# Kernel optimization log

Hardware: AMD Instinct MI355X
Metric: run time of the kernel (lower is better)

The kernel has to match this reference:

```python
import jax, jax.numpy as jnp
import numpy as np
import math

D_MODEL = 1024
D_INNER = 2048
N_HEADS = 8
D_STATE = 64
D_CONV = 4
CHUNK = 64
HEAD_DIM = D_INNER // N_HEADS
EPS = 1.1920929e-07  # torch RMSNorm default eps = finfo(fp32).eps


def _rms(x, g):
    return x * jax.lax.rsqrt(jnp.mean(x * x, axis=-1, keepdims=True) + EPS) * g


def setup_inputs() -> dict:
    key = jax.random.key(0)
    ks = jax.random.split(key, 8)
    B, S = 32, 256
    proj_out = 2 * D_INNER + 2 * N_HEADS * D_STATE + N_HEADS  # 5128
    s = 0.02
    lambdas = [0.999, 0.995, 0.99, 0.98, 0.95, 0.9, 0.8, 0.7]
    A_log = jnp.log(jnp.asarray([-math.log(l) for l in lambdas], jnp.float32))
    return {
        "hidden": jax.random.normal(ks[0], (B, S, D_MODEL), jnp.float32),
        "W_in": jax.random.normal(ks[1], (proj_out, D_MODEL), jnp.float32) * s,
        "conv_w": jax.random.normal(ks[2], (D_INNER, 1, D_CONV), jnp.float32) * 0.2,
        "conv_b": jax.random.normal(ks[3], (D_INNER,), jnp.float32) * 0.02,
        "W_dt": jax.random.normal(ks[4], (D_INNER, N_HEADS), jnp.float32) * 0.1,
        "b_dt": jax.random.normal(ks[5], (D_INNER,), jnp.float32) * 0.1,
        "A_log": A_log,
        "D": jnp.ones((N_HEADS,), jnp.float32),
        "W_out": jax.random.normal(ks[6], (D_MODEL, D_INNER), jnp.float32) * s,
        "g_in": jnp.ones((D_MODEL,), jnp.float32),
        "g_out": jnp.ones((D_INNER,), jnp.float32),
    }


def reference(hidden, W_in, conv_w, conv_b, W_dt, b_dt, A_log, D, W_out, g_in, g_out):
    B, S, _ = hidden.shape
    residual = hidden
    h = _rms(hidden, g_in)
    proj = h @ W_in.T  # [B,S,5128]
    o1, o2 = D_INNER, 2 * D_INNER
    o3 = o2 + N_HEADS * D_STATE
    o4 = o3 + N_HEADS * D_STATE
    z = proj[..., :o1]
    x = proj[..., o1:o2]
    Bf = proj[..., o2:o3]
    Cf = proj[..., o3:o4]
    dt_raw = proj[..., o4:]
    # causal depthwise conv1d (pad left d_conv-1, trim to S)
    xt = jnp.transpose(x, (0, 2, 1))  # [B, d_inner, S]
    xc = jax.lax.conv_general_dilated(
        xt, conv_w, (1,), [(D_CONV - 1, 0)],
        feature_group_count=D_INNER, dimension_numbers=("NCH", "OIH", "NCH"))
    x = jax.nn.silu(jnp.transpose(xc + conv_b[None, :, None], (0, 2, 1)))
    # dt: project 8 -> d_inner then mean over head_dim -> per-head dt
    dt = dt_raw @ W_dt.T + b_dt  # [B,S,d_inner]
    dt_h = jax.nn.softplus(dt.reshape(B, S, N_HEADS, HEAD_DIM).mean(-1))  # non-TTT path (S<384)
    Bs = Bf.reshape(B, S, N_HEADS, D_STATE)
    Cs = Cf.reshape(B, S, N_HEADS, D_STATE)
    x_h = x.reshape(B, S, N_HEADS, HEAD_DIM)
    # chunked SSD scan
    A = -jnp.exp(A_log)  # [H]
    nC, L = S // CHUNK, CHUNK
    xck = x_h.reshape(B, nC, L, N_HEADS, HEAD_DIM)
    Bck = Bs.reshape(B, nC, L, N_HEADS, D_STATE)
    Cck = Cs.reshape(B, nC, L, N_HEADS, D_STATE)
    logA = dt_h.reshape(B, nC, L, N_HEADS) * A  # [B,c,L,H]
    lcs = jnp.cumsum(logA, axis=2)
    lcs_t = jnp.transpose(lcs, (0, 1, 3, 2))  # [B,c,H,L]
    tril = jnp.tril(jnp.ones((L, L), bool))
    M = jnp.where(tril, jnp.exp(lcs_t[..., :, None] - lcs_t[..., None, :]), 0.0)  # [B,c,H,L,L]
    # intra-chunk: sum_{s<=l,n} C[l,n] M[l,s] B[s,n] x[s,d]
    G = jnp.einsum("bclhn,bcshn->bchls", Cck, Bck)
    intra = jnp.einsum("bchls,bcshd->bclhd", G * M, xck)
    # per-chunk state contributions and decays
    Mlast = jnp.exp(lcs_t[..., -1:] - lcs_t)  # [B,c,H,L] decay from step s to chunk end
    states = jnp.einsum("bchs,bcshn,bcshd->bchdn", Mlast, Bck, xck)  # [B,c,H,hD,N]
    tdec = jnp.exp(lcs[:, :, -1, :])  # [B,c,H]
    def step(hst, inp):
        td, st = inp
        return td[..., None, None] * hst + st, hst
    init = jnp.zeros((B, N_HEADS, HEAD_DIM, D_STATE), x.dtype)
    _, h0 = jax.lax.scan(step, init, (jnp.moveaxis(tdec, 1, 0), jnp.moveaxis(states, 1, 0)))
    # inter-chunk: decay(l) * C[l] . h_start
    inter = jnp.exp(lcs)[..., None] * jnp.einsum("bclhn,cbhdn->bclhd", Cck, h0)
    y = (intra + inter).reshape(B, S, N_HEADS, HEAD_DIM) + x_h * D[None, None, :, None]
    y = y.reshape(B, S, D_INNER) * jax.nn.silu(z)
    y = _rms(y, g_out)
    return residual + y @ W_out.T
```

## Files before the change

kernel.cpp:

```cpp
#include <hip/hip_runtime.h>
#include <hip/hip_bf16.h>
#include <math.h>

typedef __hip_bfloat16 bf16;
typedef __attribute__((ext_vector_type(8))) short short8;
typedef __attribute__((ext_vector_type(4))) float f32x4;

#define AS1 __attribute__((address_space(1)))
#define AS3 __attribute__((address_space(3)))

#define D_MODEL 1024
#define D_INNER 2048
#define N_HEADS 8
#define D_STATE 64
#define CHUNK 64
#define HEAD_DIM 256
#define NCHUNK 4
#define BATCH 32
#define SEQ 256
#define ROWS (BATCH*SEQ)
#define PROJ_N 5128
#define PROJ_NPAD 5376
#define O1 D_INNER
#define O2 (2*D_INNER)
#define O3 (O2 + N_HEADS*D_STATE)
#define O4 (O3 + N_HEADS*D_STATE)
#define EPSF 1.1920929e-07f

__device__ __forceinline__ float silu_f(float x){ return x / (1.0f + expf(-x)); }
__device__ __forceinline__ float b2f(bf16 v){ return __bfloat162float(v); }
__device__ __forceinline__ bf16  f2b(float v){ return __float2bfloat16(v); }
__device__ __forceinline__ short f2s(float v){ bf16 b = __float2bfloat16(v); union{bf16 b; short s;} u; u.b=b; return u.s; }
__device__ __forceinline__ float s2f(short v){ union{short s; bf16 b;} u; u.s=v; return __bfloat162float(u.b); }

__device__ __forceinline__ void gl16(const void* g, void* l){
    __builtin_amdgcn_global_load_lds((const AS1 void*)g, (AS3 void*)l, 16, 0, 0);
}

__device__ __forceinline__ float block_sum_256(float v){
    __shared__ float sm[4];
    #pragma unroll
    for (int o = 32; o > 0; o >>= 1) v += __shfl_down(v, o, 64);
    int lane = threadIdx.x & 63, w = threadIdx.x >> 6;
    if (lane == 0) sm[w] = v;
    __syncthreads();
    return sm[0] + sm[1] + sm[2] + sm[3];
}

__global__ __launch_bounds__(256) void k_rms_in(const float* __restrict__ x,
                                                const float* __restrict__ g,
                                                bf16* __restrict__ out){
    int row = blockIdx.x, t = threadIdx.x;
    const float4* xr = (const float4*)(x + (size_t)row * D_MODEL);
    float4 v = xr[t];
    float ss = v.x*v.x + v.y*v.y + v.z*v.z + v.w*v.w;
    ss = block_sum_256(ss);
    float sc = rsqrtf(ss * (1.0f/(float)D_MODEL) + EPSF);
    float4 gv = ((const float4*)g)[t];
    union { ushort4 u; bf16 b[4]; } o;
    o.b[0] = f2b(v.x*sc*gv.x); o.b[1] = f2b(v.y*sc*gv.y);
    o.b[2] = f2b(v.z*sc*gv.z); o.b[3] = f2b(v.w*sc*gv.w);
    ((ushort4*)(out + (size_t)row * D_MODEL))[t] = o.u;
}

#define N1 (PROJ_NPAD*D_MODEL)
__global__ __launch_bounds__(256) void k_cvt_both(const float* __restrict__ W_in,
                                                  const float* __restrict__ W_out,
                                                  const float* __restrict__ g_out,
                                                  bf16* __restrict__ Wb1,
                                                  bf16* __restrict__ Wb2){
    int i = (blockIdx.x * 256 + threadIdx.x) * 4;
    union { ushort4 u; bf16 b[4]; } o;
    if (i < N1){
        int n_in = PROJ_N*D_MODEL;
        if (i + 3 < n_in){
            float4 v = *(const float4*)(W_in + i);
            o.b[0]=f2b(v.x); o.b[1]=f2b(v.y); o.b[2]=f2b(v.z); o.b[3]=f2b(v.w);
        } else {
            #pragma unroll
            for (int j = 0; j < 4; j++) o.b[j] = f2b((i+j < n_in) ? W_in[i+j] : 0.f);
        }
        *(ushort4*)(Wb1 + i) = o.u;
    } else {
        int k2 = i - N1;
        if (k2 < D_MODEL*D_INNER){
            float4 v = *(const float4*)(W_out + k2);
            float4 gv = *(const float4*)(g_out + (k2 & (D_INNER-1)));
            o.b[0]=f2b(v.x*gv.x); o.b[1]=f2b(v.y*gv.y); o.b[2]=f2b(v.z*gv.z); o.b[3]=f2b(v.w*gv.w);
            *(ushort4*)(Wb2 + k2) = o.u;
        }
    }
}


__device__ __forceinline__ short8 ld32(const short* base, int row, int g){
    int sr = row >> 1;
    int e8 = (((row & 1) << 2) | g) ^ (sr & 7);
    return *(const short8*)(base + sr*64 + e8*8);
}

__device__ __forceinline__ void stage_u(const bf16* __restrict__ Ag,
                                        const bf16* __restrict__ Bg,
                                        int K, size_t bm, size_t bn, int t,
                                        short* buf, int j){
    const int tid = threadIdx.x;
    const int wid = tid >> 6;
    int cidx = j*512 + tid;
    int srow = cidx >> 3, s8 = cidx & 7;
    int eff = s8 ^ (srow & 7);
    int grow = srow*2 + (eff >> 2);
    int gcol = t*32 + (eff & 3)*8;
    const bf16* src = (grow < 256)
        ? Ag + (bm + grow) * (size_t)K + gcol
        : Bg + (bn + grow - 256) * (size_t)K + gcol;
    gl16(src, buf + (size_t)(j*512 + wid*64)*8);
}

#define MFMA_BF16(A_,B_,C_) __builtin_amdgcn_mfma_f32_16x16x32_bf16(A_,B_,C_,0,0,0)

__device__ __forceinline__ void gemm_main(const bf16* __restrict__ Ag,
                                          const bf16* __restrict__ Bg,
                                          int K, size_t bm, size_t bn,
                                          short* lds, f32x4 (&acc)[4][4]){
    constexpr int TILE = 384*32;
    const int NT = K >> 5;
    const int lane = threadIdx.x & 63;
    const int wid = threadIdx.x >> 6;
    const int wm = wid >> 1, wn = wid & 1;
    const int fr = lane & 15, g = lane >> 4;

    #pragma unroll
    for (int j = 0; j < 3; j++) stage_u(Ag, Bg, K, bm, bn, 0, lds, j);
    #pragma unroll
    for (int j = 0; j < 3; j++) stage_u(Ag, Bg, K, bm, bn, 1, lds + TILE, j);
    asm volatile("s_waitcnt vmcnt(3)" ::: "memory");
    __builtin_amdgcn_sched_barrier(0);
    __builtin_amdgcn_s_barrier();
    __builtin_amdgcn_sched_barrier(0);

    int cur = 0;
    for (int t = 0; t < NT; t++){
        short* buf = lds + cur*TILE;
        int sg = cur + 2; if (sg >= 3) sg -= 3;
        short* stg = lds + sg*TILE;
        short8 a[4], b[4];
        #pragma unroll
        for (int m = 0; m < 4; m++) a[m] = ld32(buf, wm*64 + m*16 + fr, g);
        #pragma unroll
        for (int n = 0; n < 4; n++) b[n] = ld32(buf, 256 + wn*64 + n*16 + fr, g);
        if (t + 2 < NT){
            stage_u(Ag, Bg, K, bm, bn, t+2, stg, 0);
            stage_u(Ag, Bg, K, bm, bn, t+2, stg, 1);
            stage_u(Ag, Bg, K, bm, bn, t+2, stg, 2);
        }
        __builtin_amdgcn_s_setprio(1);
        #pragma unroll
        for (int m = 0; m < 4; m++)
            #pragma unroll
            for (int n = 0; n < 4; n++)
                acc[m][n] = MFMA_BF16(a[m], b[n], acc[m][n]);
        __builtin_amdgcn_s_setprio(0);
        __builtin_amdgcn_sched_barrier(0);
        if (t + 2 < NT)      asm volatile("s_waitcnt vmcnt(3)" ::: "memory");
        else if (t + 1 < NT) asm volatile("s_waitcnt vmcnt(0)" ::: "memory");
        __builtin_amdgcn_sched_barrier(0);
        __builtin_amdgcn_s_barrier();
        __builtin_amdgcn_sched_barrier(0);
        cur = cur + 1 == 3 ? 0 : cur + 1;
    }
}

__global__ __launch_bounds__(512, 4) void k_gemm1_g(const bf16* __restrict__ A,
                                                    const bf16* __restrict__ B,
                                                    bf16* __restrict__ z,
                                                    bf16* __restrict__ xp,
                                                    bf16* __restrict__ Bc,
                                                    bf16* __restrict__ Cc,
                                                    float* __restrict__ dtr){
    extern __shared__ short lds[];
    int wg = (blockIdx.x & 7)*168 + (blockIdx.x >> 3);
    int grp = wg / 192, rem = wg % 192;
    int nt_ = grp*6 + rem % 6;
    int mt_ = rem / 6;
    size_t bm = (size_t)mt_ * 256;
    size_t bn = (size_t)nt_ * 128;
    f32x4 acc[4][4] = {};
    gemm_main(A, B, D_MODEL, bm, bn, lds, acc);
    const int lane = threadIdx.x & 63;
    const int wid = threadIdx.x >> 6;
    const int wm = wid >> 1, wn = wid & 1;
    int cr = (lane >> 4)*4, cc = lane & 15;
    #pragma unroll
    for (int m = 0; m < 4; m++){
        size_t r0 = bm + wm*64 + m*16 + cr;
        #pragma unroll
        for (int n = 0; n < 4; n++){
            int c = (int)bn + wn*64 + n*16 + cc;
            #pragma unroll
            for (int j = 0; j < 4; j++){
                float v = acc[m][n][j];
                size_t r = r0 + j;
                if (c < O1)            z  [r * D_INNER + c]        = f2b(v);
                else if (c < O2)       xp [r * D_INNER + (c - O1)] = f2b(v);
                else if (c < O3)       Bc [r * 512 + (c - O2)]     = f2b(v);
                else if (c < O4)       Cc [r * 512 + (c - O3)]     = f2b(v);
                else if (c < PROJ_N)   dtr[r * 8 + (c - O4)]       = v;
            }
        }
    }
}

__global__ __launch_bounds__(512, 4) void k_gemm2_g(const bf16* __restrict__ A,
                                                    const bf16* __restrict__ B,
                                                    const float* __restrict__ res,
                                                    float* __restrict__ C){
    extern __shared__ short lds[];
    int wg = (blockIdx.x & 7)*32 + (blockIdx.x >> 3);
    size_t bm = (size_t)(wg >> 3) * 256;
    size_t bn = (size_t)(wg & 7) * 128;
    f32x4 acc[4][4] = {};
    gemm_main(A, B, D_INNER, bm, bn, lds, acc);
    const int lane = threadIdx.x & 63;
    const int wid = threadIdx.x >> 6;
    const int wm = wid >> 1, wn = wid & 1;
    int cr = (lane >> 4)*4, cc = lane & 15;
    #pragma unroll
    for (int m = 0; m < 4; m++){
        size_t r0 = bm + wm*64 + m*16 + cr;
        #pragma unroll
        for (int n = 0; n < 4; n++){
            size_t c = bn + wn*64 + n*16 + cc;
            #pragma unroll
            for (int j = 0; j < 4; j++){
                size_t r = r0 + j;
                C[r * D_MODEL + c] = acc[m][n][j] + res[r * D_MODEL + c];
            }
        }
    }
}

__global__ __launch_bounds__(256) void k_conv_silu(const bf16* __restrict__ xp,
                                                   const float* __restrict__ cw,
                                                   const float* __restrict__ cb,
                                                   bf16* __restrict__ xout){
    int b = blockIdx.x;
    int c = blockIdx.y * 256 + threadIdx.x;
    int s0 = blockIdx.z * 32;
    float w0 = cw[c*4+0], w1 = cw[c*4+1], w2 = cw[c*4+2], w3 = cw[c*4+3];
    float bias = cb[c];
    const bf16* ib = xp + (size_t)b * SEQ * D_INNER + c;
    bf16* ob = xout + (size_t)b * SEQ * D_INNER + c;
    float x0 = 0.f, x1 = 0.f, x2 = 0.f;
    if (s0 >= 3){
        x0 = b2f(ib[(size_t)(s0-3) * D_INNER]);
        x1 = b2f(ib[(size_t)(s0-2) * D_INNER]);
        x2 = b2f(ib[(size_t)(s0-1) * D_INNER]);
    }
    #pragma unroll 4
    for (int s = s0; s < s0 + 32; s++){
        float x3 = b2f(ib[(size_t)s * D_INNER]);
        float a = x0*w0 + x1*w1 + x2*w2 + x3*w3 + bias;
        ob[(size_t)s * D_INNER] = f2b(silu_f(a));
        x0 = x1; x1 = x2; x2 = x3;
    }
}

__global__ __launch_bounds__(64) void k_dt_lcs(const float* __restrict__ dtr,
                                               const float* __restrict__ W_dt,
                                               const float* __restrict__ b_dt,
                                               const float* __restrict__ A_log,
                                               float* __restrict__ lcs,
                                               float* __restrict__ tdec){
    __shared__ float sm[80];
    __shared__ float la[CHUNK][N_HEADS];
    int bc = blockIdx.x;
    int l = threadIdx.x;
    {
        int h = l >> 3, k = l & 7;
        float s = 0.f;
        for (int d = 0; d < HEAD_DIM; d++) s += W_dt[(size_t)(h*HEAD_DIM + d) * N_HEADS + k];
        sm[l] = s * (1.0f/(float)HEAD_DIM);
        if (l < 8){
            float sb = 0.f;
            for (int d = 0; d < HEAD_DIM; d++) sb += b_dt[l*HEAD_DIM + d];
            sm[64 + l] = sb * (1.0f/(float)HEAD_DIM);
            sm[72 + l] = -expf(A_log[l]);
        }
    }
    __syncthreads();
    const float* dr = dtr + (size_t)(bc*CHUNK + l) * 8;
    float d0 = dr[0], d1 = dr[1], d2 = dr[2], d3 = dr[3];
    float d4 = dr[4], d5 = dr[5], d6 = dr[6], d7 = dr[7];
    #pragma unroll
    for (int h = 0; h < 8; h++){
        float dt = sm[64+h]
                 + d0*sm[h*8+0] + d1*sm[h*8+1] + d2*sm[h*8+2] + d3*sm[h*8+3]
                 + d4*sm[h*8+4] + d5*sm[h*8+5] + d6*sm[h*8+6] + d7*sm[h*8+7];
        float sp = (dt > 20.f) ? dt : log1pf(expf(dt));
        la[l][h] = sp * sm[72+h];
    }
    __syncthreads();
    float out[8];
    #pragma unroll
    for (int h = 0; h < 8; h++) out[h] = 0.f;
    for (int l2 = 0; l2 <= l; l2++){
        #pragma unroll
        for (int h = 0; h < 8; h++) out[h] += la[l2][h];
    }
    float* lo = lcs + (size_t)(bc*CHUNK + l) * N_HEADS;
    #pragma unroll
    for (int h = 0; h < 8; h++) lo[h] = out[h];
    if (l == 63){
        #pragma unroll
        for (int h = 0; h < 8; h++) tdec[bc*N_HEADS + h] = expf(out[h]);
    }
}

#define LB   0
#define LC   4096
#define LGM  8192
#define LXT  12800
#define LSH  29184
#define LF   45568
#define LDS_BYTES 91904

__device__ __forceinline__ short8 frag_sw(const short* arr, int r, int k){
    return *(const short8*)(arr + r*64 + (k ^ ((r&7)<<3)));
}

__global__ __launch_bounds__(256, 1) void k_ssm(const bf16* __restrict__ Bc,
                                                const bf16* __restrict__ Cc,
                                                bf16* xg,
                                                const float* __restrict__ lcs,
                                                const float* __restrict__ tdec,
                                                const float* __restrict__ Dv){
    extern __shared__ short lds[];
    short* Blds  = lds + LB;
    short* Clds  = lds + LC;
    short* GMlds = lds + LGM;
    short* XTlds = lds + LXT;
    short* Shr   = lds + LSH;
    float* el = (float*)(lds + LF);
    float* ml = el + 64;
    float* ee = el + 128;

    const int tid = threadIdx.x;
    const int lane = tid & 63;
    const int wid = tid >> 6;
    const int fr = lane & 15;
    const int fk = (lane >> 4) * 8;
    const int r0 = (lane >> 4) * 4;
    const int b = blockIdx.x >> 3, h = blockIdx.x & 7;
    const float Dh = Dv[h];

    f32x4 carry[4][4] = {};

    for (int c = 0; c < NCHUNK; c++){
        const int bc = b*NCHUNK + c;
        __syncthreads();
        #pragma unroll
        for (int i = 0; i < 2; i++){
            int slot = i*256 + tid;
            int s = slot >> 3, u = slot & 7;
            size_t rb = (size_t)(bc*CHUNK + s) * 512 + h*64 + ((u ^ (s&7)) * 8);
            gl16(Bc + rb, Blds + slot*8);
            gl16(Cc + rb, Clds + slot*8);
        }
        #pragma unroll
        for (int i = 0; i < 8; i++){
            int slot = i*256 + tid;
            int s = slot >> 5, ck = slot & 31;
            gl16(xg + (size_t)(bc*CHUNK + s) * D_INNER + h*HEAD_DIM + ck*8, Shr + slot*8);
        }
        if (tid < 64) el[tid] = lcs[(size_t)(bc*CHUNK + tid) * N_HEADS + h];
        __syncthreads();
        if (tid < 64){
            float e63 = el[63];
            ml[tid] = expf(e63 - el[tid]);
            ee[tid] = expf(el[tid]);
        }
        #pragma unroll
        for (int i = 0; i < 8; i++){
            short8 t8;
            #pragma unroll
            for (int j = 0; j < 8; j++) t8[j] = Shr[(i*8 + j)*HEAD_DIM + tid];
            *(short8*)(XTlds + tid*64 + ((i*8) ^ ((tid&7)<<3))) = t8;
        }
        __syncthreads();
        {
            f32x4 accg[4] = {};
            #pragma unroll
            for (int kk = 0; kk < 2; kk++){
                short8 a = frag_sw(Clds, wid*16 + fr, kk*32 + fk);
                #pragma unroll
                for (int nt = 0; nt < 4; nt++){
                    short8 bb = frag_sw(Blds, nt*16 + fr, kk*32 + fk);
                    accg[nt] = __builtin_amdgcn_mfma_f32_16x16x32_bf16(a, bb, accg[nt], 0, 0, 0);
                }
            }
            #pragma unroll
            for (int nt = 0; nt < 4; nt++){
                int s = nt*16 + fr;
                float els = el[s];
                #pragma unroll
                for (int j = 0; j < 4; j++){
                    int l = wid*16 + r0 + j;
                    float f = (s <= l) ? expf(el[l] - els) : 0.f;
                    GMlds[l*72 + s] = f2s(accg[nt][j] * f);
                }
            }
            int crow = wid*16 + (lane >> 2), cq = lane & 3;
            float fe = ee[crow];
            #pragma unroll
            for (int half = 0; half < 2; half++){
                short8 v = *(short8*)(Clds + crow*64 + cq*16 + half*8);
                #pragma unroll
                for (int j = 0; j < 8; j++) v[j] = f2s(s2f(v[j]) * fe);
                *(short8*)(Clds + crow*64 + cq*16 + half*8) = v;
            }
        }
        #pragma unroll
        for (int mt = 0; mt < 4; mt++)
            #pragma unroll
            for (int nt = 0; nt < 4; nt++)
                #pragma unroll
                for (int j = 0; j < 4; j++){
                    int d = wid*64 + mt*16 + r0 + j;
                    int n = nt*16 + fr;
                    Shr[d*64 + (n ^ ((d&7)<<3))] = f2s(carry[mt][nt][j]);
                }
        float btv[16];
        {
            int bn_ = tid & 63, bq = tid >> 6;
            #pragma unroll
            for (int i = 0; i < 16; i++){
                int s = bq*16 + i;
                btv[i] = s2f(Blds[s*64 + (bn_ ^ ((s&7)<<3))]) * ml[s];
            }
        }
        __syncthreads();
        {
            int bn_ = tid & 63, bq = tid >> 6;
            #pragma unroll
            for (int i = 0; i < 16; i++){
                int s = bq*16 + i;
                Blds[bn_*64 + (s ^ ((bn_&7)<<3))] = f2s(btv[i]);
            }
        }
        {
            f32x4 accy[4][4] = {};
            #pragma unroll
            for (int kk = 0; kk < 2; kk++){
                short8 ag[4], ae[4], bx[4], bh[4];
                #pragma unroll
                for (int mt = 0; mt < 4; mt++){
                    ag[mt] = *(const short8*)(GMlds + (mt*16 + fr)*72 + kk*32 + fk);
                    ae[mt] = frag_sw(Clds, mt*16 + fr, kk*32 + fk);
                }
                #pragma unroll
                for (int nt = 0; nt < 4; nt++){
                    int d = wid*64 + nt*16 + fr;
                    bx[nt] = frag_sw(XTlds, d, kk*32 + fk);
                    bh[nt] = frag_sw(Shr,  d, kk*32 + fk);
                }
                #pragma unroll
                for (int mt = 0; mt < 4; mt++)
                    #pragma unroll
                    for (int nt = 0; nt < 4; nt++){
                        accy[mt][nt] = __builtin_amdgcn_mfma_f32_16x16x32_bf16(ag[mt], bx[nt], accy[mt][nt], 0, 0, 0);
                        accy[mt][nt] = __builtin_amdgcn_mfma_f32_16x16x32_bf16(ae[mt], bh[nt], accy[mt][nt], 0, 0, 0);
                    }
            }
            #pragma unroll
            for (int mt = 0; mt < 4; mt++)
                #pragma unroll
                for (int nt = 0; nt < 4; nt++){
                    int d = wid*64 + nt*16 + fr;
                    #pragma unroll
                    for (int j = 0; j < 4; j++){
                        int l = mt*16 + r0 + j;
                        float xv = s2f(XTlds[d*64 + (l ^ ((d&7)<<3))]);
                        xg[(size_t)(bc*CHUNK + l) * D_INNER + h*HEAD_DIM + d] = f2b(accy[mt][nt][j] + xv*Dh);
                    }
                }
        }
        __syncthreads();
        {
            f32x4 accs[4][4] = {};
            #pragma unroll
            for (int kk = 0; kk < 2; kk++){
                short8 ax[4], bt[4];
                #pragma unroll
                for (int mt = 0; mt < 4; mt++)
                    ax[mt] = frag_sw(XTlds, wid*64 + mt*16 + fr, kk*32 + fk);
                #pragma unroll
                for (int nt = 0; nt < 4; nt++)
                    bt[nt] = frag_sw(Blds, nt*16 + fr, kk*32 + fk);
                #pragma unroll
                for (int mt = 0; mt < 4; mt++)
                    #pragma unroll
                    for (int nt = 0; nt < 4; nt++)
                        accs[mt][nt] = __builtin_amdgcn_mfma_f32_16x16x32_bf16(ax[mt], bt[nt], accs[mt][nt], 0, 0, 0);
            }
            float td = tdec[bc*N_HEADS + h];
            #pragma unroll
            for (int mt = 0; mt < 4; mt++)
                #pragma unroll
                for (int nt = 0; nt < 4; nt++)
                    carry[mt][nt] = td * carry[mt][nt] + accs[mt][nt];
        }
    }
}

__global__ __launch_bounds__(256) void k_gate_rms(const bf16* __restrict__ y,
                                                  const bf16* __restrict__ z,
                                                  bf16* __restrict__ yn){
    int row = blockIdx.x, t = threadIdx.x;
    union { uint4 u; bf16 b[8]; } yv, zv, ov;
    yv.u = ((const uint4*)(y + (size_t)row * D_INNER))[t];
    zv.u = ((const uint4*)(z + (size_t)row * D_INNER))[t];
    float v[8];
    float ss = 0.f;
    #pragma unroll
    for (int i = 0; i < 8; i++){
        float a = b2f(yv.b[i]);
        float q = b2f(zv.b[i]);
        v[i] = a * silu_f(q);
        ss += v[i]*v[i];
    }
    ss = block_sum_256(ss);
    float sc = rsqrtf(ss * (1.0f/(float)D_INNER) + EPSF);
    #pragma unroll
    for (int i = 0; i < 8; i++) ov.b[i] = f2b(v[i]*sc);
    ((uint4*)(yn + (size_t)row * D_INNER))[t] = ov.u;
}

extern "C" void kernel_launch(void* const* d_in, const int* in_sizes, int n_in,
                              void* d_out, int out_size, void* d_ws, size_t ws_size,
                              hipStream_t stream){
    const float* hidden = (const float*)d_in[0];
    const float* W_in   = (const float*)d_in[1];
    const float* conv_w = (const float*)d_in[2];
    const float* conv_b = (const float*)d_in[3];
    const float* W_dt   = (const float*)d_in[4];
    const float* b_dt   = (const float*)d_in[5];
    const float* A_log  = (const float*)d_in[6];
    const float* Dv     = (const float*)d_in[7];
    const float* W_out  = (const float*)d_in[8];
    const float* g_in   = (const float*)d_in[9];
    const float* g_out  = (const float*)d_in[10];

    char* ws = (char*)d_ws;
    bf16*  z    = (bf16*)(ws + 0);
    bf16*  xp   = (bf16*)(ws + 33554432);
    bf16*  x    = (bf16*)(ws + 67108864);
    bf16*  Bc   = (bf16*)(ws + 100663296);
    bf16*  Cc   = (bf16*)(ws + 109051904);
    float* dtr  = (float*)(ws + 117440512);
    float* lcs  = (float*)(ws + 117702656);
    float* tdec = (float*)(ws + 117964800);
    bf16*  Wb1  = (bf16*)(ws + 117969408);
    bf16*  hnb  = (bf16*)(ws + 128979456);
    bf16*  Wb2  = (bf16*)(ws + 145756672);
    bf16*  yn   = xp;

    k_rms_in<<<ROWS, 256, 0, stream>>>(hidden, g_in, hnb);
    k_cvt_both<<<(N1 + D_MODEL*D_INNER)/1024, 256, 0, stream>>>(W_in, W_out, g_out, Wb1, Wb2);
    hipFuncSetAttribute((const void*)k_gemm1_g, hipFuncAttributeMaxDynamicSharedMemorySize, 73728);
    k_gemm1_g<<<(ROWS/256)*(PROJ_NPAD/128), 512, 73728, stream>>>(hnb, Wb1, z, xp, Bc, Cc, dtr);
    k_conv_silu<<<dim3(BATCH, D_INNER/256, SEQ/32), 256, 0, stream>>>(xp, conv_w, conv_b, x);
    k_dt_lcs<<<BATCH*NCHUNK, 64, 0, stream>>>(dtr, W_dt, b_dt, A_log, lcs, tdec);
    hipFuncSetAttribute((const void*)k_ssm, hipFuncAttributeMaxDynamicSharedMemorySize, LDS_BYTES);
    k_ssm<<<BATCH*N_HEADS, 256, LDS_BYTES, stream>>>(Bc, Cc, x, lcs, tdec, Dv);
    k_gate_rms<<<ROWS, 256, 0, stream>>>(x, z, yn);
    hipFuncSetAttribute((const void*)k_gemm2_g, hipFuncAttributeMaxDynamicSharedMemorySize, 73728);
    k_gemm2_g<<<(ROWS/256)*(D_MODEL/128), 512, 73728, stream>>>(yn, Wb2, hidden, (float*)d_out);
}
```

Before: 265.4 us.

## Rewrite input projection GEMM as 256x256 tile with ping-pong staged pipeline

```diff
diff --git a/kernel.cpp b/kernel.cpp
--- a/kernel.cpp
+++ b/kernel.cpp
@@ -92,11 +92,21 @@
     }
 }
 
-
 __device__ __forceinline__ short8 ld32(const short* base, int row, int g){
     int sr = row >> 1;
     int e8 = (((row & 1) << 2) | g) ^ (sr & 7);
     return *(const short8*)(base + sr*64 + e8*8);
+}
+
+__device__ __forceinline__ void stage_h(const bf16* __restrict__ G, size_t brow,
+                                        int K, int gcol0, short* region, int j){
+    const int tid = threadIdx.x, wid = tid >> 6;
+    int cidx = j*512 + tid;
+    int srow = cidx >> 3, s8 = cidx & 7;
+    int eff = s8 ^ (srow & 7);
+    int grow = srow*2 + (eff >> 2);
+    int gcol = gcol0 + (eff & 3)*8;
+    gl16(G + (brow + grow)*(size_t)K + gcol, region + (size_t)(j*512 + wid*64)*8);
 }
 
 __device__ __forceinline__ void stage_u(const bf16* __restrict__ Ag,
@@ -117,6 +127,7 @@
 }
 
 #define MFMA_BF16(A_,B_,C_) __builtin_amdgcn_mfma_f32_16x16x32_bf16(A_,B_,C_,0,0,0)
+#define SB __builtin_amdgcn_sched_barrier(0)
 
 __device__ __forceinline__ void gemm_main(const bf16* __restrict__ Ag,
                                           const bf16* __restrict__ Bg,
@@ -134,9 +145,7 @@
     #pragma unroll
     for (int j = 0; j < 3; j++) stage_u(Ag, Bg, K, bm, bn, 1, lds + TILE, j);
     asm volatile("s_waitcnt vmcnt(3)" ::: "memory");
-    __builtin_amdgcn_sched_barrier(0);
-    __builtin_amdgcn_s_barrier();
-    __builtin_amdgcn_sched_barrier(0);
+    SB; __builtin_amdgcn_s_barrier(); SB;
 
     int cur = 0;
     for (int t = 0; t < NT; t++){
@@ -160,39 +169,113 @@
             for (int n = 0; n < 4; n++)
                 acc[m][n] = MFMA_BF16(a[m], b[n], acc[m][n]);
         __builtin_amdgcn_s_setprio(0);
-        __builtin_amdgcn_sched_barrier(0);
+        SB;
         if (t + 2 < NT)      asm volatile("s_waitcnt vmcnt(3)" ::: "memory");
         else if (t + 1 < NT) asm volatile("s_waitcnt vmcnt(0)" ::: "memory");
-        __builtin_amdgcn_sched_barrier(0);
-        __builtin_amdgcn_s_barrier();
-        __builtin_amdgcn_sched_barrier(0);
+        SB; __builtin_amdgcn_s_barrier(); SB;
         cur = cur + 1 == 3 ? 0 : cur + 1;
     }
 }
 
-__global__ __launch_bounds__(512, 4) void k_gemm1_g(const bf16* __restrict__ A,
-                                                    const bf16* __restrict__ B,
-                                                    bf16* __restrict__ z,
-                                                    bf16* __restrict__ xp,
-                                                    bf16* __restrict__ Bc,
-                                                    bf16* __restrict__ Cc,
-                                                    float* __restrict__ dtr){
+__global__ __launch_bounds__(512, 1) void k_gemm1_p4(const bf16* __restrict__ A,
+                                                     const bf16* __restrict__ B,
+                                                     bf16* __restrict__ z,
+                                                     bf16* __restrict__ xp,
+                                                     bf16* __restrict__ Bc,
+                                                     bf16* __restrict__ Cc,
+                                                     float* __restrict__ dtr){
     extern __shared__ short lds[];
-    int wg = (blockIdx.x & 7)*168 + (blockIdx.x >> 3);
-    int grp = wg / 192, rem = wg % 192;
-    int nt_ = grp*6 + rem % 6;
-    int mt_ = rem / 6;
+    int wg = (blockIdx.x & 7)*84 + (blockIdx.x >> 3);
+    int nt_ = wg / 32, mt_ = wg % 32;
     size_t bm = (size_t)mt_ * 256;
-    size_t bn = (size_t)nt_ * 128;
-    f32x4 acc[4][4] = {};
-    gemm_main(A, B, D_MODEL, bm, bn, lds, acc);
-    const int lane = threadIdx.x & 63;
-    const int wid = threadIdx.x >> 6;
-    const int wm = wid >> 1, wn = wid & 1;
+    size_t bn = (size_t)nt_ * 256;
+    const int lane = threadIdx.x & 63, wid = threadIdx.x >> 6;
+    const int wm = wid >> 2, wn = wid & 3;
+    const int fr = lane & 15, g = lane >> 4;
+    constexpr int NT = D_MODEL / 64;
+    f32x4 acc[8][4] = {};
+
+    #define AK(d,kh) (lds + (d)*32768 + (kh)*8192)
+    #define BK_(d,kh) (lds + (d)*32768 + 16384 + (kh)*8192)
+    #define STG_A(tt,kh,d) do{ stage_h(A, bm, D_MODEL, (tt)*64+(kh)*32, AK(d,kh), 0); \
+                               stage_h(A, bm, D_MODEL, (tt)*64+(kh)*32, AK(d,kh), 1);}while(0)
+    #define STG_B(tt,kh,d) do{ stage_h(B, bn, D_MODEL, (tt)*64+(kh)*32, BK_(d,kh), 0); \
+                               stage_h(B, bn, D_MODEL, (tt)*64+(kh)*32, BK_(d,kh), 1);}while(0)
+
+    STG_A(0,0,0); STG_B(0,0,0);
+    STG_A(0,1,0); STG_B(0,1,0);
+    STG_A(1,0,1); STG_B(1,0,1);
+    asm volatile("s_waitcnt vmcnt(8)" ::: "memory");
+    SB; __builtin_amdgcn_s_barrier(); SB;
+
+    for (int t = 0; t < NT; t++){
+        const int d = t & 1, dn = d ^ 1;
+        short *A0 = AK(d,0), *A1 = AK(d,1), *B0 = BK_(d,0), *B1 = BK_(d,1);
+        short8 a[4], b[4];
+        #pragma unroll
+        for (int m = 0; m < 4; m++) a[m] = ld32(A0, wm*128 + m*16 + fr, g);
+        #pragma unroll
+        for (int n = 0; n < 4; n++) b[n] = ld32(B0, wn*64 + n*16 + fr, g);
+        if (t + 1 < NT) STG_A(t+1, 1, dn);
+        SB; __builtin_amdgcn_s_barrier(); SB;
+        __builtin_amdgcn_s_setprio(1);
+        #pragma unroll
+        for (int m = 0; m < 4; m++)
+            #pragma unroll
+            for (int n = 0; n < 4; n++)
+                acc[m][n] = MFMA_BF16(a[m], b[n], acc[m][n]);
+        __builtin_amdgcn_s_setprio(0);
+        SB; __builtin_amdgcn_s_barrier(); SB;
+        #pragma unroll
+        for (int m = 0; m < 4; m++) a[m] = ld32(A0, wm*128 + 64 + m*16 + fr, g);
+        if (t + 1 < NT) STG_B(t+1, 1, dn);
+        SB; __builtin_amdgcn_s_barrier(); SB;
+        __builtin_amdgcn_s_setprio(1);
+        #pragma unroll
+        for (int m = 0; m < 4; m++)
+            #pragma unroll
+            for (int n = 0; n < 4; n++)
+                acc[4+m][n] = MFMA_BF16(a[m], b[n], acc[4+m][n]);
+        __builtin_amdgcn_s_setprio(0);
+        SB;
+        if (t == NT-1) asm volatile("s_waitcnt vmcnt(0)" ::: "memory");
+        else           asm volatile("s_waitcnt vmcnt(8)" ::: "memory");
+        SB; __builtin_amdgcn_s_barrier(); SB;
+        #pragma unroll
+        for (int m = 0; m < 4; m++) a[m] = ld32(A1, wm*128 + m*16 + fr, g);
+        #pragma unroll
+        for (int n = 0; n < 4; n++) b[n] = ld32(B1, wn*64 + n*16 + fr, g);
+        if (t + 2 < NT) STG_A(t+2, 0, d);
+        SB; __builtin_amdgcn_s_barrier(); SB;
+        __builtin_amdgcn_s_setprio(1);
+        #pragma unroll
+        for (int m = 0; m < 4; m++)
+            #pragma unroll
+            for (int n = 0; n < 4; n++)
+                acc[m][n] = MFMA_BF16(a[m], b[n], acc[m][n]);
+        __builtin_amdgcn_s_setprio(0);
+        SB; __builtin_amdgcn_s_barrier(); SB;
+        #pragma unroll
+        for (int m = 0; m < 4; m++) a[m] = ld32(A1, wm*128 + 64 + m*16 + fr, g);
+        if (t + 2 < NT) STG_B(t+2, 0, d);
+        SB; __builtin_amdgcn_s_barrier(); SB;
+        __builtin_amdgcn_s_setprio(1);
+        #pragma unroll
+        for (int m = 0; m < 4; m++)
+            #pragma unroll
+            for (int n = 0; n < 4; n++)
+                acc[4+m][n] = MFMA_BF16(a[m], b[n], acc[4+m][n]);
+        __builtin_amdgcn_s_setprio(0);
+        SB;
+        if (t < NT-2)       asm volatile("s_waitcnt vmcnt(8)" ::: "memory");
+        else if (t == NT-2) asm volatile("s_waitcnt vmcnt(4)" ::: "memory");
+        SB; __builtin_amdgcn_s_barrier(); SB;
+    }
+
     int cr = (lane >> 4)*4, cc = lane & 15;
     #pragma unroll
-    for (int m = 0; m < 4; m++){
-        size_t r0 = bm + wm*64 + m*16 + cr;
+    for (int m = 0; m < 8; m++){
+        size_t r0 = bm + wm*128 + m*16 + cr;
         #pragma unroll
         for (int n = 0; n < 4; n++){
             int c = (int)bn + wn*64 + n*16 + cc;
@@ -208,6 +291,10 @@
             }
         }
     }
+    #undef AK
+    #undef BK_
+    #undef STG_A
+    #undef STG_B
 }
 
 __global__ __launch_bounds__(512, 4) void k_gemm2_g(const bf16* __restrict__ A,
@@ -566,8 +653,8 @@
 
     k_rms_in<<<ROWS, 256, 0, stream>>>(hidden, g_in, hnb);
     k_cvt_both<<<(N1 + D_MODEL*D_INNER)/1024, 256, 0, stream>>>(W_in, W_out, g_out, Wb1, Wb2);
-    hipFuncSetAttribute((const void*)k_gemm1_g, hipFuncAttributeMaxDynamicSharedMemorySize, 73728);
-    k_gemm1_g<<<(ROWS/256)*(PROJ_NPAD/128), 512, 73728, stream>>>(hnb, Wb1, z, xp, Bc, Cc, dtr);
+    hipFuncSetAttribute((const void*)k_gemm1_p4, hipFuncAttributeMaxDynamicSharedMemorySize, 131072);
+    k_gemm1_p4<<<(ROWS/256)*(PROJ_NPAD/256), 512, 131072, stream>>>(hnb, Wb1, z, xp, Bc, Cc, dtr);
     k_conv_silu<<<dim3(BATCH, D_INNER/256, SEQ/32), 256, 0, stream>>>(xp, conv_w, conv_b, x);
     k_dt_lcs<<<BATCH*NCHUNK, 64, 0, stream>>>(dtr, W_dt, b_dt, A_log, lcs, tdec);
     hipFuncSetAttribute((const void*)k_ssm, hipFuncAttributeMaxDynamicSharedMemorySize, LDS_BYTES);
```

Result: slower. 349.2 us (+31.5%).
